# Kernel optimization log

Hardware: AMD Instinct MI355X
Metric: run time of the kernel (lower is better)

Reference implementation:

```python
import jax, jax.numpy as jnp
import numpy as np

# Mamba2 hyperparams (mamba_ssm defaults given __init__ args)
D_MODEL = 512
FF = 2048
D_STATE = 128
D_CONV = 4
EXPAND = 2
D_INNER = EXPAND * D_MODEL          # 1024
HEADDIM = 64
NHEADS = D_INNER // HEADDIM         # 16
NGROUPS = 1
CONV_DIM = D_INNER + 2 * NGROUPS * D_STATE       # 1280
D_IN_PROJ = 2 * D_INNER + 2 * NGROUPS * D_STATE + NHEADS  # 2320
CHUNK = 128
EPS = 1e-5


def setup_inputs() -> dict:
    key = jax.random.key(0)
    ks = jax.random.split(key, 16)
    B, S = 8, 2048
    s = 0.02
    dt_init = jax.random.uniform(ks[4], (NHEADS,), minval=0.001, maxval=0.1)
    return {
        # forward args (dropout treated as eval / identity)
        "tgt": jax.random.normal(ks[0], (B, S, D_MODEL), jnp.float32),
        "memory": jax.random.normal(ks[1], (B, 256, D_MODEL), jnp.float32),
        "spatial_shapes": jnp.array([[16, 16]], jnp.int32),
        "level_start_index": jnp.array([0], jnp.int32),
        "valid_ratios": jnp.ones((B, 1, 2), jnp.float32),
        # Mamba2 params
        "in_proj_w": jax.random.normal(ks[2], (D_IN_PROJ, D_MODEL), jnp.float32) * s,
        "conv_w": jax.random.normal(ks[3], (CONV_DIM, D_CONV), jnp.float32) * s,
        "conv_b": jnp.zeros((CONV_DIM,), jnp.float32),
        "dt_bias": jnp.log(jnp.expm1(dt_init)),  # inverse softplus of dt_init
        "A_log": jnp.log(jax.random.uniform(ks[5], (NHEADS,), minval=1.0, maxval=16.0)),
        "D_head": jnp.ones((NHEADS,), jnp.float32),
        "norm_w": jnp.ones((D_INNER,), jnp.float32),
        "out_proj_w": jax.random.normal(ks[6], (D_MODEL, D_INNER), jnp.float32) * s,
        # LayerNorms + FFN
        "norm1_w": jnp.ones((D_MODEL,)), "norm1_b": jnp.zeros((D_MODEL,)),
        "w1": jax.random.normal(ks[7], (FF, D_MODEL), jnp.float32) * s,
        "b1": jnp.zeros((FF,)),
        "w2": jax.random.normal(ks[8], (D_MODEL, FF), jnp.float32) * s,
        "b2": jnp.zeros((D_MODEL,)),
        "norm3_w": jnp.ones((D_MODEL,)), "norm3_b": jnp.zeros((D_MODEL,)),
    }


def _layer_norm(x, w, b):
    m = jnp.mean(x, -1, keepdims=True)
    v = jnp.mean((x - m) ** 2, -1, keepdims=True)
    return (x - m) * jax.lax.rsqrt(v + EPS) * w + b


def _ssd(x, dt, A, Bm, Cm):
    # chunked selective-scan (SSD). x:(b,s,h,p) dt:(b,s,h) A:(h,) Bm,Cm:(b,s,n)
    b, s, h, p = x.shape
    n = Bm.shape[-1]
    c, l = s // CHUNK, CHUNK
    x = x.reshape(b, c, l, h, p)
    dt = dt.reshape(b, c, l, h)
    Bm = Bm.reshape(b, c, l, n)
    Cm = Cm.reshape(b, c, l, n)
    a_cs = jnp.cumsum(dt * A, axis=2)                 # (b,c,l,h) cumulative log-decay
    ac = a_cs.transpose(0, 1, 3, 2)                   # (b,c,h,l)
    mask = jnp.tril(jnp.ones((l, l), bool))
    Lmat = jnp.exp(jnp.where(mask, ac[..., :, None] - ac[..., None, :], -jnp.inf))
    # intra-chunk (causal) contribution
    Y_diag = jnp.einsum('bcin,bcjn,bchij,bcjh,bcjhp->bcihp', Cm, Bm, Lmat, dt, x)
    # per-chunk final states
    decay_end = jnp.exp(a_cs[:, :, -1:, :] - a_cs)    # (b,c,l,h)
    states = jnp.einsum('bcln,bclh,bclh,bclhp->bchpn', Bm, decay_end, dt, x)
    chunk_decay = jnp.exp(a_cs[:, :, -1, :])          # (b,c,h)
    def step(h0, inp):
        cd, st = inp
        return cd[:, :, None, None] * h0 + st, h0
    h_init = jnp.zeros((b, h, p, n), x.dtype)
    _, prev = jax.lax.scan(step, h_init,
                           (chunk_decay.transpose(1, 0, 2),
                            states.transpose(1, 0, 2, 3, 4)))
    prev = prev.transpose(1, 0, 2, 3, 4)              # (b,c,h,p,n) state at chunk start
    Y_off = jnp.einsum('bcln,bchpn,bclh->bclhp', Cm, prev, jnp.exp(a_cs))
    return (Y_diag + Y_off).reshape(b, s, h, p)


def _mamba2(u, in_proj_w, conv_w, conv_b, dt_bias, A_log, D_head, norm_w, out_proj_w):
    Bb, S, _ = u.shape
    zxbcdt = u @ in_proj_w.T                          # (b,s,2320)
    z, xBC, dt = jnp.split(zxbcdt, [D_INNER, D_INNER + CONV_DIM], axis=-1)
    # causal depthwise conv1d + silu
    xp = jnp.pad(xBC, ((0, 0), (D_CONV - 1, 0), (0, 0)))
    conv = sum(xp[:, k:k + S, :] * conv_w[:, k] for k in range(D_CONV)) + conv_b
    xBC = jax.nn.silu(conv)
    x, Bm, Cm = jnp.split(xBC, [D_INNER, D_INNER + NGROUPS * D_STATE], axis=-1)
    dt = jax.nn.softplus(dt + dt_bias)                # (b,s,h)
    A = -jnp.exp(A_log)                               # (h,)
    x = x.reshape(Bb, S, NHEADS, HEADDIM)
    y = _ssd(x, dt, A, Bm, Cm) + D_head[None, None, :, None] * x
    y = y.reshape(Bb, S, D_INNER)
    # gated RMSNorm: rmsnorm(y * silu(z)) * w
    y = y * jax.nn.silu(z)
    y = y * jax.lax.rsqrt(jnp.mean(y * y, -1, keepdims=True) + EPS) * norm_w
    return y @ out_proj_w.T


def reference(tgt, memory, spatial_shapes, level_start_index, valid_ratios,
              in_proj_w, conv_w, conv_b, dt_bias, A_log, D_head, norm_w, out_proj_w,
              norm1_w, norm1_b, w1, b1, w2, b2, norm3_w, norm3_b):
    t2 = _mamba2(tgt, in_proj_w, conv_w, conv_b, dt_bias, A_log, D_head, norm_w, out_proj_w)
    t = _layer_norm(tgt + t2, norm1_w, norm1_b)
    ff = jax.nn.gelu(t @ w1.T + b1, approximate=False) @ w2.T + b2
    return _layer_norm(t + ff, norm3_w, norm3_b)
```

## Files before the change

### kernel.cpp

```cpp
#include <hip/hip_runtime.h>
#include <hip/hip_bf16.h>
#include <math.h>


namespace {
constexpr int BB = 8;
constexpr int S = 2048;
constexpr int DM = 512;
constexpr int DIP = 2320;
constexpr int DIPP = 2432;
constexpr int DI = 1024;
constexpr int CDIM = 1280;
constexpr int NH = 16;
constexpr int HD = 64;
constexpr int DSTATE = 128;
constexpr int CH = 128;
constexpr int NC = S / CH;
constexpr int FF = 2048;
constexpr float EPS = 1e-5f;
constexpr int LP = 132;
}

using bf16_t = __hip_bfloat16;
typedef __attribute__((ext_vector_type(8))) short short8;
typedef __attribute__((ext_vector_type(4))) float f32x4;

__device__ __forceinline__ float gelu_exact(float x) {
    return 0.5f * x * (1.0f + erff(x * 0.7071067811865476f));
}
__device__ __forceinline__ unsigned short f2bfu(float f) {
    bf16_t b = __float2bfloat16(f);
    return *(unsigned short*)&b;
}
__device__ __forceinline__ float bfu2f(unsigned short u) {
    union { unsigned int i; float f; } v; v.i = (unsigned)u << 16; return v.f;
}

__device__ __forceinline__ void gload16(const bf16_t* g, bf16_t* l) {
    __builtin_amdgcn_global_load_lds(
        (const __attribute__((address_space(1))) void*)g,
        (__attribute__((address_space(3))) void*)l, 16, 0, 0);
}

__device__ __forceinline__ void block_sum2(float& a, float& b) {
    #pragma unroll
    for (int o = 32; o > 0; o >>= 1) {
        a += __shfl_down(a, o, 64);
        b += __shfl_down(b, o, 64);
    }
    __shared__ float sa[4], sb[4];
    int w = threadIdx.x >> 6;
    if ((threadIdx.x & 63) == 0) { sa[w] = a; sb[w] = b; }
    __syncthreads();
    a = sa[0] + sa[1] + sa[2] + sa[3];
    b = sb[0] + sb[1] + sb[2] + sb[3];
}

template <int BM, int ACT, bool HASBIAS, bool OUTBF>
__global__ __launch_bounds__(256)
void mfma_gemm(const bf16_t* __restrict__ A, const bf16_t* __restrict__ W,
               const float* __restrict__ bias, void* __restrict__ Cout,
               int N, int K, int lda, int ldw, int ldc,
               long batchA, long batchW, long batchC)
{
    A += (long)blockIdx.z * batchA;
    W += (long)blockIdx.z * batchW;
    constexpr int NJ = (BM == 128) ? 4 : 2;
    __shared__ bf16_t As[2][BM * 32];
    __shared__ bf16_t Ws[2][4096];
    const int tid = threadIdx.x;
    const int lane = tid & 63;
    const int wave = tid >> 6;
    const long bm = (long)blockIdx.y * BM;
    const int bn = blockIdx.x * 128;

    const int rA = tid & (BM - 1);
    const int qA = tid / BM;
    const int rW = tid & 127;
    const int qW = tid >> 7;
    const bf16_t* Ag = A + (bm + rA) * (long)lda + qA * 8;
    const bf16_t* Wg = W + ((long)bn + rW) * (long)ldw + qW * 8;
    const int wbase = wave * 512;

    const int kq = lane >> 4;
    const int lr = lane & 15;
    const int wm = (BM == 128) ? (wave & 1) * 64 : 0;
    const int wn = (BM == 128) ? (wave >> 1) * 64 : wave * 32;

    f32x4 acc[4][NJ];
    #pragma unroll
    for (int i = 0; i < 4; i++)
        #pragma unroll
        for (int j = 0; j < NJ; j++) acc[i][j] = (f32x4){0.f, 0.f, 0.f, 0.f};

    {
        gload16(Ag, &As[0][wbase]);
        if (BM == 128) gload16(Ag + 16, &As[0][wbase + 2048]);
        gload16(Wg, &Ws[0][wbase]);
        gload16(Wg + 16, &Ws[0][wbase + 2048]);
    }
    __syncthreads();

    const int nt = K / 32;
    for (int t = 0; t < nt; t++) {
        const int cur = t & 1, nxt = cur ^ 1;
        if (t + 1 < nt) {
            const int ko = (t + 1) * 32;
            gload16(Ag + ko, &As[nxt][wbase]);
            if (BM == 128) gload16(Ag + ko + 16, &As[nxt][wbase + 2048]);
            gload16(Wg + ko, &Ws[nxt][wbase]);
            gload16(Wg + ko + 16, &Ws[nxt][wbase + 2048]);
        }
        short8 af[4], bfr[NJ];
        #pragma unroll
        for (int i = 0; i < 4; i++)
            af[i] = *(const short8*)&As[cur][(kq * BM + wm + i * 16 + lr) * 8];
        #pragma unroll
        for (int j = 0; j < NJ; j++)
            bfr[j] = *(const short8*)&Ws[cur][(kq * 128 + wn + j * 16 + lr) * 8];
        #pragma unroll
        for (int i = 0; i < 4; i++)
            #pragma unroll
            for (int j = 0; j < NJ; j++)
                acc[i][j] = __builtin_amdgcn_mfma_f32_16x16x32_bf16(af[i], bfr[j], acc[i][j], 0, 0, 0);
        __syncthreads();
    }

    #pragma unroll
    for (int i = 0; i < 4; i++) {
        #pragma unroll
        for (int j = 0; j < NJ; j++) {
            int col = bn + wn + j * 16 + lr;
            if (col < N) {
                float bv = HASBIAS ? bias[col] : 0.f;
                #pragma unroll
                for (int r = 0; r < 4; r++) {
                    long row = bm + wm + i * 16 + kq * 4 + r;
                    float v = acc[i][j][r] + bv;
                    if (ACT == 1) v = gelu_exact(v);
                    if (OUTBF) ((bf16_t*)Cout)[row * (long)ldc + col + blockIdx.z * batchC] = __float2bfloat16(v);
                    else       ((float*)Cout)[row * (long)ldc + col + blockIdx.z * batchC] = v;
                }
            }
        }
    }
}

template <int ACT, bool HASBIAS>
__global__ __launch_bounds__(256)
void gemm_kernel(const float* __restrict__ A, const float* __restrict__ W,
                 const float* __restrict__ bias, float* __restrict__ C,
                 int M, int N, int K, int lda, int ldw, int ldc,
                 long batchA, long batchW, long batchC)
{
    A += (long)blockIdx.z * batchA;
    W += (long)blockIdx.z * batchW;
    C += (long)blockIdx.z * batchC;
    __shared__ __align__(16) float Asm[16][68];
    __shared__ __align__(16) float Wsm[16][68];
    const int tid = threadIdx.x;
    const int bm = blockIdx.y * 64;
    const int bn = blockIdx.x * 64;
    const int tm = (tid & 15) * 4;
    const int tn = (tid >> 4) * 4;
    const int lr = tid >> 2;
    const int lk = (tid & 3) * 4;
    const float* Ap = A + (long)(bm + lr) * lda + lk;
    const float* Wp = W + (long)(bn + lr) * ldw + lk;
    const bool wv_ok = (bn + lr) < N;
    float acc[4][4];
    #pragma unroll
    for (int i = 0; i < 4; i++)
        #pragma unroll
        for (int j = 0; j < 4; j++) acc[i][j] = 0.f;

    for (int k0 = 0; k0 < K; k0 += 16) {
        float4 av = *(const float4*)(Ap + k0);
        float4 wv = wv_ok ? *(const float4*)(Wp + k0) : make_float4(0.f, 0.f, 0.f, 0.f);
        Asm[lk + 0][lr] = av.x; Asm[lk + 1][lr] = av.y;
        Asm[lk + 2][lr] = av.z; Asm[lk + 3][lr] = av.w;
        Wsm[lk + 0][lr] = wv.x; Wsm[lk + 1][lr] = wv.y;
        Wsm[lk + 2][lr] = wv.z; Wsm[lk + 3][lr] = wv.w;
        __syncthreads();
        #pragma unroll
        for (int k = 0; k < 16; k++) {
            float4 a = *(const float4*)&Asm[k][tm];
            float4 w = *(const float4*)&Wsm[k][tn];
            acc[0][0] += a.x * w.x; acc[0][1] += a.x * w.y; acc[0][2] += a.x * w.z; acc[0][3] += a.x * w.w;
            acc[1][0] += a.y * w.x; acc[1][1] += a.y * w.y; acc[1][2] += a.y * w.z; acc[1][3] += a.y * w.w;
            acc[2][0] += a.z * w.x; acc[2][1] += a.z * w.y; acc[2][2] += a.z * w.z; acc[2][3] += a.z * w.w;
            acc[3][0] += a.w * w.x; acc[3][1] += a.w * w.y; acc[3][2] += a.w * w.z; acc[3][3] += a.w * w.w;
        }
        __syncthreads();
    }
    #pragma unroll
    for (int i = 0; i < 4; i++) {
        long row = bm + tm + i;
        #pragma unroll
        for (int j = 0; j < 4; j++) {
            int col = bn + tn + j;
            if (col < N) {
                float v = acc[i][j];
                if (HASBIAS) v += bias[col];
                if (ACT == 1) v = gelu_exact(v);
                if (ACT == 2) v = (v > 20.f) ? v : log1pf(__expf(v));
                C[row * ldc + col] = v;
            }
        }
    }
}

__global__ __launch_bounds__(256)
void cvt_bf16(const float* __restrict__ s, bf16_t* __restrict__ d, long n)
{
    long i = ((long)blockIdx.x * 256 + threadIdx.x) * 4;
    if (i >= n) return;
    float4 v = *(const float4*)(s + i);
    d[i + 0] = __float2bfloat16(v.x);
    d[i + 1] = __float2bfloat16(v.y);
    d[i + 2] = __float2bfloat16(v.z);
    d[i + 3] = __float2bfloat16(v.w);
}

__global__ __launch_bounds__(256)
void cvt_bf16_pad(const float* __restrict__ s, bf16_t* __restrict__ d,
                  int rows_src, long total, int cols)
{
    long i = (long)blockIdx.x * 256 + threadIdx.x;
    if (i >= total) return;
    long r = i / cols;
    d[i] = __float2bfloat16(r < rows_src ? s[i] : 0.f);
}

__global__ __launch_bounds__(256)
void conv_silu_t16(const bf16_t* __restrict__ zx, const float* __restrict__ cw,
                   const float* __restrict__ cb, bf16_t* __restrict__ xBC)
{
    const int quad = blockIdx.x * 64 + (threadIdx.x & 63);
    const int wv = threadIdx.x >> 6;
    const int c = quad * 4;
    const int s0 = blockIdx.y * 64 + wv * 16;
    const long t0 = (long)blockIdx.z * S + s0;

    float wgt[4][4];
    #pragma unroll
    for (int cc = 0; cc < 4; cc++)
        #pragma unroll
        for (int k = 0; k < 4; k++) wgt[cc][k] = cw[(c + cc) * 4 + k];
    float bias[4];
    #pragma unroll
    for (int cc = 0; cc < 4; cc++) bias[cc] = cb[c + cc];

    unsigned long long rows[19];
    #pragma unroll
    for (int i = 0; i < 19; i++) {
        int s = s0 + i - 3;
        rows[i] = (s >= 0) ? *(const unsigned long long*)&zx[(t0 + i - 3) * DIP + DI + c] : 0ULL;
    }
    #pragma unroll
    for (int i = 0; i < 16; i++) {
        float v[4];
        #pragma unroll
        for (int cc = 0; cc < 4; cc++) v[cc] = bias[cc];
        #pragma unroll
        for (int k = 0; k < 4; k++) {
            unsigned long long u = rows[i + k];
            v[0] += bfu2f((unsigned short)(u      )) * wgt[0][k];
            v[1] += bfu2f((unsigned short)(u >> 16)) * wgt[1][k];
            v[2] += bfu2f((unsigned short)(u >> 32)) * wgt[2][k];
            v[3] += bfu2f((unsigned short)(u >> 48)) * wgt[3][k];
        }
        unsigned long long o = 0;
        #pragma unroll
        for (int cc = 0; cc < 4; cc++) {
            float sv = v[cc] / (1.f + __expf(-v[cc]));
            o |= (unsigned long long)f2bfu(sv) << (16 * cc);
        }
        *(unsigned long long*)&xBC[(t0 + i) * (long)CDIM + c] = o;
    }
}

__global__ __launch_bounds__(256)
void ssd_states(const bf16_t* __restrict__ xBC, const float* __restrict__ dts,
                const float* __restrict__ A_log,
                float* __restrict__ st, float* __restrict__ acs_all,
                float* __restrict__ cdlog)
{
    const int bid = blockIdx.x;
    const int nh = bid & 1;
    const int h = (bid >> 1) & 15;
    const int c = (bid >> 5) & 15;
    const int b = bid >> 9;
    const int sbid = (b * NC + c) * NH + h;
    const int tid = threadIdx.x;
    const int lane = tid & 63;
    const int wave = tid >> 6;
    __shared__ float dtv[128];
    __shared__ float acs[128];
    __shared__ float wj[128];
    __shared__ bf16_t XT[64 * LP];
    __shared__ bf16_t BwT[64 * LP];
    const long t0 = (long)b * S + (long)c * CH;
    const float Ah = -__expf(A_log[h]);

    if (tid < 128) {
        float d = dts[(t0 + tid) * NH + h];
        dtv[tid] = d;
        acs[tid] = d * Ah;
    }
    __syncthreads();
    for (int off = 1; off < 128; off <<= 1) {
        float add = 0.f;
        if (tid < 128 && tid >= off) add = acs[tid - off];
        __syncthreads();
        if (tid < 128 && tid >= off) acs[tid] += add;
        __syncthreads();
    }
    const float el = acs[127];
    if (tid < 128) wj[tid] = __expf(el - acs[tid]) * dtv[tid];
    if (nh == 0) {
        if (tid < 128) acs_all[(long)sbid * 128 + tid] = acs[tid];
        if (tid == 0) cdlog[sbid] = el;
    }
    __syncthreads();

    const int n0b = nh * 64;
    for (int i = tid; i < 4096; i += 256) {
        int p = i & 63, jp = (i >> 6) << 1;
        unsigned short a = *(const unsigned short*)&xBC[(t0 + jp) * CDIM + h * HD + p];
        unsigned short bb = *(const unsigned short*)&xBC[(t0 + jp + 1) * CDIM + h * HD + p];
        *(unsigned int*)&XT[p * LP + jp] = (unsigned)a | ((unsigned)bb << 16);
    }
    for (int i = tid; i < 4096; i += 256) {
        int n = i & 63, jp = (i >> 6) << 1;
        float v0 = __bfloat162float(xBC[(t0 + jp) * CDIM + DI + n0b + n]) * wj[jp];
        float v1 = __bfloat162float(xBC[(t0 + jp + 1) * CDIM + DI + n0b + n]) * wj[jp + 1];
        *(unsigned int*)&BwT[n * LP + jp] = (unsigned)f2bfu(v0) | ((unsigned)f2bfu(v1) << 16);
    }
    __syncthreads();

    const int kq = lane >> 4;
    const int lr = lane & 15;
    const int p0w = (wave & 1) * 32;
    const int n0w = (wave >> 1) * 32;
    f32x4 acc[2][2];
    #pragma unroll
    for (int i = 0; i < 2; i++)
        #pragma unroll
        for (int j = 0; j < 2; j++) acc[i][j] = (f32x4){0.f, 0.f, 0.f, 0.f};
    #pragma unroll
    for (int t = 0; t < 4; t++) {
        short8 af[2], bfr[2];
        #pragma unroll
        for (int i = 0; i < 2; i++)
            af[i] = *(const short8*)&XT[(p0w + i * 16 + lr) * LP + t * 32 + kq * 8];
        #pragma unroll
        for (int j = 0; j < 2; j++)
            bfr[j] = *(const short8*)&BwT[(n0w + j * 16 + lr) * LP + t * 32 + kq * 8];
        #pragma unroll
        for (int i = 0; i < 2; i++)
            #pragma unroll
            for (int j = 0; j < 2; j++)
                acc[i][j] = __builtin_amdgcn_mfma_f32_16x16x32_bf16(af[i], bfr[j], acc[i][j], 0, 0, 0);
    }
    long base = (long)sbid * 8192;
    #pragma unroll
    for (int i = 0; i < 2; i++)
        #pragma unroll
        for (int j = 0; j < 2; j++) {
            int col = n0b + n0w + j * 16 + lr;
            #pragma unroll
            for (int r = 0; r < 4; r++) {
                int p = p0w + i * 16 + kq * 4 + r;
                st[base + p * 128 + col] = acc[i][j][r];
            }
        }
}

__global__ __launch_bounds__(256)
void ssd_scan(float* __restrict__ st, const float* __restrict__ cdlog)
{
    const int h = blockIdx.x & 15;
    const int b = blockIdx.x >> 4;
    const int q0 = blockIdx.y * 8;
    const int tid = threadIdx.x;
    float prev[8];
    #pragma unroll
    for (int q = 0; q < 8; q++) prev[q] = 0.f;
    for (int c = 0; c < NC; c++) {
        int bc = (b * NC + c) * NH + h;
        float cd = __expf(cdlog[bc]);
        long base = (long)bc * 8192 + (long)q0 * 256;
        #pragma unroll
        for (int q = 0; q < 8; q++) {
            long idx = base + (long)q * 256 + tid;
            float v = st[idx];
            st[idx] = prev[q];
            prev[q] = cd * prev[q] + v;
        }
    }
}

__global__ __launch_bounds__(256)
void ssd_out(const bf16_t* __restrict__ xBC, const float* __restrict__ dts,
             const bf16_t* __restrict__ G, const float* __restrict__ st,
             const float* __restrict__ acs_all, const float* __restrict__ D_head,
             bf16_t* __restrict__ y)
{
    const int bid = blockIdx.x;
    const int ih = bid & 1;
    const int h = (bid >> 1) & 15;
    const int c = (bid >> 5) & 15;
    const int b = bid >> 9;
    const int sbid = (b * NC + c) * NH + h;
    const int tid = threadIdx.x;
    const int lane = tid & 63;
    const int wave = tid >> 6;
    __shared__ float dtv[128];
    __shared__ float acs[128];
    __shared__ float eacs[64];
    __shared__ bf16_t Abuf[64 * LP];
    __shared__ bf16_t Bbuf[64 * LP];
    const long t0 = (long)b * S + (long)c * CH;
    const int m0b = ih * 64;

    if (tid < 128) {
        dtv[tid] = dts[(t0 + tid) * NH + h];
        acs[tid] = acs_all[(long)sbid * 128 + tid];
    }
    __syncthreads();
    if (tid < 64) eacs[tid] = __expf(acs[m0b + tid]);

    const bf16_t* Gb = G + (long)(b * NC + c) * 128 * 128;
    for (int i = tid; i < 4096; i += 256) {
        int rl = i >> 6, kp = (i & 63) << 1;
        int grow = m0b + rl;
        unsigned int g2 = *(const unsigned int*)&Gb[grow * 128 + kp];
        float w0 = (kp     <= grow) ? bfu2f((unsigned short)(g2      )) * __expf(acs[grow] - acs[kp    ]) * dtv[kp    ] : 0.f;
        float w1 = (kp + 1 <= grow) ? bfu2f((unsigned short)(g2 >> 16)) * __expf(acs[grow] - acs[kp + 1]) * dtv[kp + 1] : 0.f;
        *(unsigned int*)&Abuf[rl * LP + kp] = (unsigned)f2bfu(w0) | ((unsigned)f2bfu(w1) << 16);
    }
    for (int i = tid; i < 4096; i += 256) {
        int p = i & 63, jp = (i >> 6) << 1;
        unsigned short a = *(const unsigned short*)&xBC[(t0 + jp) * CDIM + h * HD + p];
        unsigned short bb = *(const unsigned short*)&xBC[(t0 + jp + 1) * CDIM + h * HD + p];
        *(unsigned int*)&Bbuf[p * LP + jp] = (unsigned)a | ((unsigned)bb << 16);
    }
    __syncthreads();

    const int kq = lane >> 4;
    const int lr = lane & 15;
    const int m0w = (wave & 1) * 32;
    const int p0 = (wave >> 1) * 32;
    f32x4 acc[2][2];
    #pragma unroll
    for (int i = 0; i < 2; i++)
        #pragma unroll
        for (int j = 0; j < 2; j++) acc[i][j] = (f32x4){0.f, 0.f, 0.f, 0.f};

    #pragma unroll
    for (int t = 0; t < 4; t++) {
        short8 af[2], bfr[2];
        #pragma unroll
        for (int i = 0; i < 2; i++)
            af[i] = *(const short8*)&Abuf[(m0w + i * 16 + lr) * LP + t * 32 + kq * 8];
        #pragma unroll
        for (int j = 0; j < 2; j++)
            bfr[j] = *(const short8*)&Bbuf[(p0 + j * 16 + lr) * LP + t * 32 + kq * 8];
        #pragma unroll
        for (int i = 0; i < 2; i++)
            #pragma unroll
            for (int j = 0; j < 2; j++)
                acc[i][j] = __builtin_amdgcn_mfma_f32_16x16x32_bf16(af[i], bfr[j], acc[i][j], 0, 0, 0);
    }
    const float Dh = D_head[h];
    float dx[2][2][4];
    #pragma unroll
    for (int i = 0; i < 2; i++)
        #pragma unroll
        for (int j = 0; j < 2; j++) {
            int col = p0 + j * 16 + lr;
            #pragma unroll
            for (int r = 0; r < 4; r++) {
                int rl = m0w + i * 16 + kq * 4 + r;
                dx[i][j][r] = Dh * __bfloat162float(Bbuf[col * LP + m0b + rl]);
            }
        }
    __syncthreads();

    for (int i = tid; i < 4096; i += 256) {
        int rl = i >> 6, np = (i & 63) << 1;
        unsigned int c2 = *(const unsigned int*)&xBC[(t0 + m0b + rl) * CDIM + DI + DSTATE + np];
        float e = eacs[rl];
        float v0 = e * bfu2f((unsigned short)(c2      ));
        float v1 = e * bfu2f((unsigned short)(c2 >> 16));
        *(unsigned int*)&Abuf[rl * LP + np] = (unsigned)f2bfu(v0) | ((unsigned)f2bfu(v1) << 16);
    }
    for (int i = tid; i < 4096; i += 256) {
        int p = i >> 6, np = (i & 63) << 1;
        float2 v = *(const float2*)&st[(long)sbid * 8192 + p * 128 + np];
        *(unsigned int*)&Bbuf[p * LP + np] = (unsigned)f2bfu(v.x) | ((unsigned)f2bfu(v.y) << 16);
    }
    __syncthreads();

    #pragma unroll
    for (int t = 0; t < 4; t++) {
        short8 af[2], bfr[2];
        #pragma unroll
        for (int i = 0; i < 2; i++)
            af[i] = *(const short8*)&Abuf[(m0w + i * 16 + lr) * LP + t * 32 + kq * 8];
        #pragma unroll
        for (int j = 0; j < 2; j++)
            bfr[j] = *(const short8*)&Bbuf[(p0 + j * 16 + lr) * LP + t * 32 + kq * 8];
        #pragma unroll
        for (int i = 0; i < 2; i++)
            #pragma unroll
            for (int j = 0; j < 2; j++)
                acc[i][j] = __builtin_amdgcn_mfma_f32_16x16x32_bf16(af[i], bfr[j], acc[i][j], 0, 0, 0);
    }

    #pragma unroll
    for (int i = 0; i < 2; i++)
        #pragma unroll
        for (int j = 0; j < 2; j++) {
            int col = p0 + j * 16 + lr;
            #pragma unroll
            for (int r = 0; r < 4; r++) {
                int rl = m0w + i * 16 + kq * 4 + r;
                y[(t0 + m0b + rl) * DI + h * HD + col] = __float2bfloat16(acc[i][j][r] + dx[i][j][r]);
            }
        }
}

__global__ __launch_bounds__(256)
void gated_rms(const bf16_t* __restrict__ y, const bf16_t* __restrict__ zx,
               const float* __restrict__ norm_w, bf16_t* __restrict__ yn)
{
    const long t = blockIdx.x;
    const int d = threadIdx.x * 4;
    unsigned long long zu = *(const unsigned long long*)&zx[t * DIP + d];
    unsigned long long yu = *(const unsigned long long*)&y[t * DI + d];
    float g[4];
    float ss = 0.f, dummy = 0.f;
    #pragma unroll
    for (int q = 0; q < 4; q++) {
        float zv = bfu2f((unsigned short)(zu >> (16 * q)));
        float yv = bfu2f((unsigned short)(yu >> (16 * q)));
        float gv = yv * (zv / (1.f + __expf(-zv)));
        g[q] = gv;
        ss += gv * gv;
    }
    block_sum2(ss, dummy);
    float scale = rsqrtf(ss * (1.f / DI) + EPS);
    unsigned long long o = 0;
    #pragma unroll
    for (int q = 0; q < 4; q++)
        o |= (unsigned long long)f2bfu(g[q] * scale * norm_w[d + q]) << (16 * q);
    *(unsigned long long*)&yn[t * DI + d] = o;
}

template <bool W16>
__global__ __launch_bounds__(256)
void add_ln(const float* __restrict__ x, const float* __restrict__ r,
            const float* __restrict__ w, const float* __restrict__ bpar,
            float* __restrict__ o32, bf16_t* __restrict__ o16)
{
    const int tid = threadIdx.x;
    const long t = blockIdx.x * 2 + (tid >> 7);
    const int i = (tid & 127) * 4;
    float4 xv = *(const float4*)(x + t * DM + i);
    float4 rv = *(const float4*)(r + t * DM + i);
    float v[4] = {xv.x + rv.x, xv.y + rv.y, xv.z + rv.z, xv.w + rv.w};
    float s = v[0] + v[1] + v[2] + v[3];
    float s2 = v[0]*v[0] + v[1]*v[1] + v[2]*v[2] + v[3]*v[3];
    #pragma unroll
    for (int o = 32; o > 0; o >>= 1) {
        s += __shfl_down(s, o, 64);
        s2 += __shfl_down(s2, o, 64);
    }
    __shared__ float sa[4], sb[4];
    int wv = tid >> 6;
    if ((tid & 63) == 0) { sa[wv] = s; sb[wv] = s2; }
    __syncthreads();
    int base = (tid >> 7) * 2;
    s = sa[base] + sa[base + 1];
    s2 = sb[base] + sb[base + 1];
    float mean = s * (1.f / DM);
    float var = s2 * (1.f / DM) - mean * mean;
    float inv = rsqrtf(var + EPS);
    float4 ov;
    float* op = (float*)&ov;
    unsigned long long o16u = 0;
    #pragma unroll
    for (int q = 0; q < 4; q++) {
        float o = (v[q] - mean) * inv * w[i + q] + bpar[i + q];
        op[q] = o;
        if (W16) o16u |= (unsigned long long)f2bfu(o) << (16 * q);
    }
    *(float4*)(o32 + t * DM + i) = ov;
    if (W16) *(unsigned long long*)&o16[t * DM + i] = o16u;
}


extern "C" void kernel_launch(void* const* d_in, const int* in_sizes, int n_in,
                              void* d_out, int out_size, void* d_ws, size_t ws_size,
                              hipStream_t stream)
{
    const float* tgt       = (const float*)d_in[0];
    const float* in_proj_w = (const float*)d_in[5];
    const float* conv_w    = (const float*)d_in[6];
    const float* conv_b    = (const float*)d_in[7];
    const float* dt_bias   = (const float*)d_in[8];
    const float* A_log     = (const float*)d_in[9];
    const float* D_head    = (const float*)d_in[10];
    const float* norm_w    = (const float*)d_in[11];
    const float* out_proj_w= (const float*)d_in[12];
    const float* norm1_w   = (const float*)d_in[13];
    const float* norm1_b   = (const float*)d_in[14];
    const float* w1        = (const float*)d_in[15];
    const float* b1        = (const float*)d_in[16];
    const float* w2        = (const float*)d_in[17];
    const float* b2        = (const float*)d_in[18];
    const float* norm3_w   = (const float*)d_in[19];
    const float* norm3_b   = (const float*)d_in[20];
    float* out = (float*)d_out;

    float* ws = (float*)d_ws;

    const size_t SZ_INW  = (size_t)DIPP * DM / 2;
    const size_t SZ_OUTW = (size_t)DM * DI / 2;
    const size_t SZ_W1   = (size_t)FF * DM / 2;
    const size_t SZ_W2   = (size_t)DM * FF / 2;
    size_t wo = 0;
    bf16_t* inW  = (bf16_t*)(ws + wo); wo += SZ_INW;
    bf16_t* outW = (bf16_t*)(ws + wo); wo += SZ_OUTW;
    bf16_t* w1b  = (bf16_t*)(ws + wo); wo += SZ_W1;
    bf16_t* w2b  = (bf16_t*)(ws + wo); wo += SZ_W2;
    const size_t WB = wo;

    const size_t PB = (size_t)S * DM / 2
                    + (size_t)S * DIP / 2
                    + (size_t)S * NH
                    + (size_t)S * CDIM / 2
                    + (size_t)NC * 128 * 128 / 2
                    + (size_t)NC * NH * 128
                    + (size_t)NC * NH
                    + (size_t)S * DI
                    + (size_t)S * DI;
    int NB = 0;
    for (int nb = 8; nb >= 1; nb >>= 1) {
        if (ws_size >= (WB + (size_t)nb * PB) * sizeof(float)) { NB = nb; break; }
    }
    if (NB == 0) return;

    {
        long n = (long)DIPP * DM;
        cvt_bf16_pad<<<(n + 255) / 256, 256, 0, stream>>>(in_proj_w, inW, DIP, n, DM);
        n = (long)DM * DI;
        cvt_bf16<<<(n / 4 + 255) / 256, 256, 0, stream>>>(out_proj_w, outW, n);
        n = (long)FF * DM;
        cvt_bf16<<<(n / 4 + 255) / 256, 256, 0, stream>>>(w1, w1b, n);
        n = (long)DM * FF;
        cvt_bf16<<<(n / 4 + 255) / 256, 256, 0, stream>>>(w2, w2b, n);
    }

    for (int b0 = 0; b0 < BB; b0 += NB) {
        const long Tg = (long)NB * S;
        size_t o = WB;
        bf16_t* tgt_bf = (bf16_t*)(ws + o); o += (size_t)Tg * DM / 2;
        bf16_t* zx     = (bf16_t*)(ws + o); o += (size_t)Tg * DIP / 2;
        float*  dts    = ws + o;            o += (size_t)Tg * NH;
        bf16_t* xBC    = (bf16_t*)(ws + o); o += (size_t)Tg * CDIM / 2;
        bf16_t* Gbuf   = (bf16_t*)(ws + o); o += (size_t)NB * NC * 128 * 128 / 2;
        float*  acs    = ws + o;            o += (size_t)NB * NC * NH * 128;
        float*  cdl    = ws + o;            o += (size_t)NB * NC * NH;
        float*  ybuf   = ws + o;            o += (size_t)Tg * DI;
        float*  st     = ws + o;            o += (size_t)Tg * DI;

        bf16_t* ybf = (bf16_t*)ybuf;
        bf16_t* yn  = (bf16_t*)st;
        float*  t2  = ybuf;
        float*  tb  = (float*)zx;
        bf16_t* tbb = (bf16_t*)(((float*)zx) + Tg * DM);
        bf16_t* h1  = (bf16_t*)ybuf;
        float*  fb  = (float*)xBC;

        const float* tgt_g = tgt + (long)b0 * S * DM;
        float* out_g = out + (long)b0 * S * DM;

        cvt_bf16<<<((Tg * DM) / 4 + 255) / 256, 256, 0, stream>>>(tgt_g, tgt_bf, Tg * DM);
        mfma_gemm<128, 0, false, true><<<dim3(DIPP / 128, Tg / 128, 1), 256, 0, stream>>>(
            tgt_bf, inW, nullptr, zx, DIP, DM, DM, DM, DIP, 0, 0, 0);
        gemm_kernel<2, true><<<dim3(1, Tg / 64, 1), 256, 0, stream>>>(
            tgt_g, in_proj_w + (long)(DI + CDIM) * DM, dt_bias, dts,
            Tg, NH, DM, DM, DM, NH, 0, 0, 0);
        conv_silu_t16<<<dim3(CDIM / 256, S / 64, NB), 256, 0, stream>>>(zx, conv_w, conv_b, xBC);
        mfma_gemm<128, 0, false, true><<<dim3(1, 1, NB * NC), 256, 0, stream>>>(
            xBC + DI + DSTATE, xBC + DI, nullptr, Gbuf,
            128, DSTATE, CDIM, CDIM, 128,
            (long)CH * CDIM, (long)CH * CDIM, (long)128 * 128);
        ssd_states<<<NB * NC * NH * 2, 256, 0, stream>>>(xBC, dts, A_log, st, acs, cdl);
        ssd_scan<<<dim3(NB * NH, 4), 256, 0, stream>>>(st, cdl);
        ssd_out<<<NB * NC * NH * 2, 256, 0, stream>>>(xBC, dts, Gbuf, st, acs, D_head, ybf);
        gated_rms<<<Tg, 256, 0, stream>>>(ybf, zx, norm_w, yn);
        mfma_gemm<64, 0, false, false><<<dim3(DM / 128, Tg / 64, 1), 256, 0, stream>>>(
            yn, outW, nullptr, t2, DM, DI, DI, DI, DM, 0, 0, 0);
        add_ln<true><<<Tg / 2, 256, 0, stream>>>(tgt_g, t2, norm1_w, norm1_b, tb, tbb);
        mfma_gemm<128, 1, true, true><<<dim3(FF / 128, Tg / 128, 1), 256, 0, stream>>>(
            tbb, w1b, b1, h1, FF, DM, DM, DM, FF, 0, 0, 0);
        mfma_gemm<64, 0, true, false><<<dim3(DM / 128, Tg / 64, 1), 256, 0, stream>>>(
            h1, w2b, b2, fb, DM, FF, FF, FF, DM, 0, 0, 0);
        add_ln<false><<<Tg / 2, 256, 0, stream>>>(tb, fb, norm3_w, norm3_b, out_g, nullptr);
    }
}
```

Baseline: 855.4 us.

## Register-staged GEMM pipeline, fused dt projection with bf16 cast, bf16 scan states

The MFMA GEMM stops using global_load_lds and instead prefetches the next K-tile into registers, storing it to LDS after the current tile's compute, with a configurable BK (64 for the out-proj and FFN2 GEMMs, which also move to 128-row tiles). The scalar fp32 dt GEMM and the separate tgt-to-bf16 conversion kernel are merged into one warp-reduction kernel. The SSD scan now writes inter-chunk states as bf16 into a separate buffer, so ssd_out reads half the bytes and skips the conversion. Together these cut launches and memory traffic and aim to hide load latency, at the cost of more registers and LDS per block and fewer blocks for the N=512 GEMMs.

```diff
diff --git a/kernel.cpp b/kernel.cpp
--- a/kernel.cpp
+++ b/kernel.cpp
@@ -36,12 +36,6 @@
     union { unsigned int i; float f; } v; v.i = (unsigned)u << 16; return v.f;
 }
 
-__device__ __forceinline__ void gload16(const bf16_t* g, bf16_t* l) {
-    __builtin_amdgcn_global_load_lds(
-        (const __attribute__((address_space(1))) void*)g,
-        (__attribute__((address_space(3))) void*)l, 16, 0, 0);
-}
-
 __device__ __forceinline__ void block_sum2(float& a, float& b) {
     #pragma unroll
     for (int o = 32; o > 0; o >>= 1) {
@@ -56,7 +50,7 @@
     b = sb[0] + sb[1] + sb[2] + sb[3];
 }
 
-template <int BM, int ACT, bool HASBIAS, bool OUTBF>
+template <int BM, int BK, int ACT, bool HASBIAS, bool OUTBF>
 __global__ __launch_bounds__(256)
 void mfma_gemm(const bf16_t* __restrict__ A, const bf16_t* __restrict__ W,
                const float* __restrict__ bias, void* __restrict__ Cout,
@@ -66,8 +60,12 @@
     A += (long)blockIdx.z * batchA;
     W += (long)blockIdx.z * batchW;
     constexpr int NJ = (BM == 128) ? 4 : 2;
-    __shared__ bf16_t As[2][BM * 32];
-    __shared__ bf16_t Ws[2][4096];
+    constexpr int KO = BK / 32;
+    constexpr int QA = 256 / BM;
+    constexpr int TA = (BM * BK) / 2048;
+    constexpr int TW = (128 * BK) / 2048;
+    __shared__ bf16_t As[2][BM * BK];
+    __shared__ bf16_t Ws[2][128 * BK];
     const int tid = threadIdx.x;
     const int lane = tid & 63;
     const int wave = tid >> 6;
@@ -80,7 +78,8 @@
     const int qW = tid >> 7;
     const bf16_t* Ag = A + (bm + rA) * (long)lda + qA * 8;
     const bf16_t* Wg = W + ((long)bn + rW) * (long)ldw + qW * 8;
-    const int wbase = wave * 512;
+    const int laoff = (qA * BM + rA) * 8;
+    const int lwoff = (qW * 128 + rW) * 8;
 
     const int kq = lane >> 4;
     const int lr = lane & 15;
@@ -93,37 +92,48 @@
         #pragma unroll
         for (int j = 0; j < NJ; j++) acc[i][j] = (f32x4){0.f, 0.f, 0.f, 0.f};
 
-    {
-        gload16(Ag, &As[0][wbase]);
-        if (BM == 128) gload16(Ag + 16, &As[0][wbase + 2048]);
-        gload16(Wg, &Ws[0][wbase]);
-        gload16(Wg + 16, &Ws[0][wbase + 2048]);
-    }
-    __syncthreads();
-
-    const int nt = K / 32;
+    short8 ra[TA], rw[TW];
+    #pragma unroll
+    for (int u = 0; u < TA; u++) ra[u] = *(const short8*)(Ag + u * (QA * 8));
+    #pragma unroll
+    for (int u = 0; u < TW; u++) rw[u] = *(const short8*)(Wg + u * 16);
+    #pragma unroll
+    for (int u = 0; u < TA; u++) *(short8*)&As[0][laoff + u * (QA * BM * 8)] = ra[u];
+    #pragma unroll
+    for (int u = 0; u < TW; u++) *(short8*)&Ws[0][lwoff + u * 2048] = rw[u];
+
+    const int nt = K / BK;
     for (int t = 0; t < nt; t++) {
         const int cur = t & 1, nxt = cur ^ 1;
         if (t + 1 < nt) {
-            const int ko = (t + 1) * 32;
-            gload16(Ag + ko, &As[nxt][wbase]);
-            if (BM == 128) gload16(Ag + ko + 16, &As[nxt][wbase + 2048]);
-            gload16(Wg + ko, &Ws[nxt][wbase]);
-            gload16(Wg + ko + 16, &Ws[nxt][wbase + 2048]);
-        }
-        short8 af[4], bfr[NJ];
-        #pragma unroll
-        for (int i = 0; i < 4; i++)
-            af[i] = *(const short8*)&As[cur][(kq * BM + wm + i * 16 + lr) * 8];
-        #pragma unroll
-        for (int j = 0; j < NJ; j++)
-            bfr[j] = *(const short8*)&Ws[cur][(kq * 128 + wn + j * 16 + lr) * 8];
-        #pragma unroll
-        for (int i = 0; i < 4; i++)
+            const long ko = (long)(t + 1) * BK;
+            #pragma unroll
+            for (int u = 0; u < TA; u++) ra[u] = *(const short8*)(Ag + ko + u * (QA * 8));
+            #pragma unroll
+            for (int u = 0; u < TW; u++) rw[u] = *(const short8*)(Wg + ko + u * 16);
+        }
+        __syncthreads();
+        #pragma unroll
+        for (int hk = 0; hk < KO; hk++) {
+            short8 af[4], bfr[NJ];
+            #pragma unroll
+            for (int i = 0; i < 4; i++)
+                af[i] = *(const short8*)&As[cur][((hk * 4 + kq) * BM + wm + i * 16 + lr) * 8];
             #pragma unroll
             for (int j = 0; j < NJ; j++)
-                acc[i][j] = __builtin_amdgcn_mfma_f32_16x16x32_bf16(af[i], bfr[j], acc[i][j], 0, 0, 0);
-        __syncthreads();
+                bfr[j] = *(const short8*)&Ws[cur][((hk * 4 + kq) * 128 + wn + j * 16 + lr) * 8];
+            #pragma unroll
+            for (int i = 0; i < 4; i++)
+                #pragma unroll
+                for (int j = 0; j < NJ; j++)
+                    acc[i][j] = __builtin_amdgcn_mfma_f32_16x16x32_bf16(af[i], bfr[j], acc[i][j], 0, 0, 0);
+        }
+        if (t + 1 < nt) {
+            #pragma unroll
+            for (int u = 0; u < TA; u++) *(short8*)&As[nxt][laoff + u * (QA * BM * 8)] = ra[u];
+            #pragma unroll
+            for (int u = 0; u < TW; u++) *(short8*)&Ws[nxt][lwoff + u * 2048] = rw[u];
+        }
     }
 
     #pragma unroll
@@ -146,65 +156,55 @@
     }
 }
 
-template <int ACT, bool HASBIAS>
-__global__ __launch_bounds__(256)
-void gemm_kernel(const float* __restrict__ A, const float* __restrict__ W,
-                 const float* __restrict__ bias, float* __restrict__ C,
-                 int M, int N, int K, int lda, int ldw, int ldc,
-                 long batchA, long batchW, long batchC)
-{
-    A += (long)blockIdx.z * batchA;
-    W += (long)blockIdx.z * batchW;
-    C += (long)blockIdx.z * batchC;
-    __shared__ __align__(16) float Asm[16][68];
-    __shared__ __align__(16) float Wsm[16][68];
-    const int tid = threadIdx.x;
-    const int bm = blockIdx.y * 64;
-    const int bn = blockIdx.x * 64;
-    const int tm = (tid & 15) * 4;
-    const int tn = (tid >> 4) * 4;
-    const int lr = tid >> 2;
-    const int lk = (tid & 3) * 4;
-    const float* Ap = A + (long)(bm + lr) * lda + lk;
-    const float* Wp = W + (long)(bn + lr) * ldw + lk;
-    const bool wv_ok = (bn + lr) < N;
-    float acc[4][4];
-    #pragma unroll
-    for (int i = 0; i < 4; i++)
-        #pragma unroll
-        for (int j = 0; j < 4; j++) acc[i][j] = 0.f;
-
-    for (int k0 = 0; k0 < K; k0 += 16) {
-        float4 av = *(const float4*)(Ap + k0);
-        float4 wv = wv_ok ? *(const float4*)(Wp + k0) : make_float4(0.f, 0.f, 0.f, 0.f);
-        Asm[lk + 0][lr] = av.x; Asm[lk + 1][lr] = av.y;
-        Asm[lk + 2][lr] = av.z; Asm[lk + 3][lr] = av.w;
-        Wsm[lk + 0][lr] = wv.x; Wsm[lk + 1][lr] = wv.y;
-        Wsm[lk + 2][lr] = wv.z; Wsm[lk + 3][lr] = wv.w;
-        __syncthreads();
-        #pragma unroll
-        for (int k = 0; k < 16; k++) {
-            float4 a = *(const float4*)&Asm[k][tm];
-            float4 w = *(const float4*)&Wsm[k][tn];
-            acc[0][0] += a.x * w.x; acc[0][1] += a.x * w.y; acc[0][2] += a.x * w.z; acc[0][3] += a.x * w.w;
-            acc[1][0] += a.y * w.x; acc[1][1] += a.y * w.y; acc[1][2] += a.y * w.z; acc[1][3] += a.y * w.w;
-            acc[2][0] += a.z * w.x; acc[2][1] += a.z * w.y; acc[2][2] += a.z * w.z; acc[2][3] += a.z * w.w;
-            acc[3][0] += a.w * w.x; acc[3][1] += a.w * w.y; acc[3][2] += a.w * w.z; acc[3][3] += a.w * w.w;
-        }
-        __syncthreads();
-    }
-    #pragma unroll
-    for (int i = 0; i < 4; i++) {
-        long row = bm + tm + i;
-        #pragma unroll
-        for (int j = 0; j < 4; j++) {
-            int col = bn + tn + j;
-            if (col < N) {
-                float v = acc[i][j];
-                if (HASBIAS) v += bias[col];
-                if (ACT == 1) v = gelu_exact(v);
-                if (ACT == 2) v = (v > 20.f) ? v : log1pf(__expf(v));
-                C[row * ldc + col] = v;
+__global__ __launch_bounds__(256)
+void dt_cvt(const float* __restrict__ tgt, const float* __restrict__ Wdt,
+            const float* __restrict__ dt_bias, bf16_t* __restrict__ tgt_bf,
+            float* __restrict__ dts)
+{
+    const int lane = threadIdx.x & 63;
+    const int wave = threadIdx.x >> 6;
+    float Wl[16][8];
+    #pragma unroll
+    for (int h = 0; h < 16; h++) {
+        float4 a = *(const float4*)&Wdt[h * 512 + lane * 8];
+        float4 b = *(const float4*)&Wdt[h * 512 + lane * 8 + 4];
+        Wl[h][0] = a.x; Wl[h][1] = a.y; Wl[h][2] = a.z; Wl[h][3] = a.w;
+        Wl[h][4] = b.x; Wl[h][5] = b.y; Wl[h][6] = b.z; Wl[h][7] = b.w;
+    }
+    float bs[16];
+    #pragma unroll
+    for (int h = 0; h < 16; h++) bs[h] = dt_bias[h];
+
+    const long row0 = ((long)blockIdx.x * 4 + wave) * 4;
+    #pragma unroll
+    for (int rr = 0; rr < 4; rr++) {
+        const long t = row0 + rr;
+        float4 xa = *(const float4*)&tgt[t * 512 + lane * 8];
+        float4 xb = *(const float4*)&tgt[t * 512 + lane * 8 + 4];
+        float x[8] = {xa.x, xa.y, xa.z, xa.w, xb.x, xb.y, xb.z, xb.w};
+        short8 ob;
+        #pragma unroll
+        for (int q = 0; q < 8; q++) ob[q] = (short)f2bfu(x[q]);
+        *(short8*)&tgt_bf[t * 512 + lane * 8] = ob;
+
+        float acc[16];
+        #pragma unroll
+        for (int h = 0; h < 16; h++) {
+            float s = 0.f;
+            #pragma unroll
+            for (int q = 0; q < 8; q++) s += x[q] * Wl[h][q];
+            acc[h] = s;
+        }
+        #pragma unroll
+        for (int off = 32; off > 0; off >>= 1)
+            #pragma unroll
+            for (int h = 0; h < 16; h++)
+                acc[h] += __shfl_xor(acc[h], off, 64);
+        if (lane == 0) {
+            #pragma unroll
+            for (int h = 0; h < 16; h++) {
+                float v = acc[h] + bs[h];
+                dts[t * NH + h] = (v > 20.f) ? v : log1pf(__expf(v));
             }
         }
     }
@@ -378,7 +378,8 @@
 }
 
 __global__ __launch_bounds__(256)
-void ssd_scan(float* __restrict__ st, const float* __restrict__ cdlog)
+void ssd_scan(const float* __restrict__ st, const float* __restrict__ cdlog,
+              bf16_t* __restrict__ prevb)
 {
     const int h = blockIdx.x & 15;
     const int b = blockIdx.x >> 4;
@@ -395,7 +396,7 @@
         for (int q = 0; q < 8; q++) {
             long idx = base + (long)q * 256 + tid;
             float v = st[idx];
-            st[idx] = prev[q];
+            prevb[idx] = __float2bfloat16(prev[q]);
             prev[q] = cd * prev[q] + v;
         }
     }
@@ -403,7 +404,7 @@
 
 __global__ __launch_bounds__(256)
 void ssd_out(const bf16_t* __restrict__ xBC, const float* __restrict__ dts,
-             const bf16_t* __restrict__ G, const float* __restrict__ st,
+             const bf16_t* __restrict__ G, const bf16_t* __restrict__ prevb,
              const float* __restrict__ acs_all, const float* __restrict__ D_head,
              bf16_t* __restrict__ y)
 {
@@ -498,8 +499,8 @@
     }
     for (int i = tid; i < 4096; i += 256) {
         int p = i >> 6, np = (i & 63) << 1;
-        float2 v = *(const float2*)&st[(long)sbid * 8192 + p * 128 + np];
-        *(unsigned int*)&Bbuf[p * LP + np] = (unsigned)f2bfu(v.x) | ((unsigned)f2bfu(v.y) << 16);
+        *(unsigned int*)&Bbuf[p * LP + np] =
+            *(const unsigned int*)&prevb[(long)sbid * 8192 + p * 128 + np];
     }
     __syncthreads();
 
@@ -677,7 +678,8 @@
         float*  ybuf   = ws + o;            o += (size_t)Tg * DI;
         float*  st     = ws + o;            o += (size_t)Tg * DI;
 
-        bf16_t* ybf = (bf16_t*)ybuf;
+        bf16_t* ybf   = (bf16_t*)ybuf;
+        bf16_t* prevb = (bf16_t*)(ybuf + (size_t)Tg * DI / 2);
         bf16_t* yn  = (bf16_t*)st;
         float*  t2  = ybuf;
         float*  tb  = (float*)zx;
@@ -688,27 +690,25 @@
         const float* tgt_g = tgt + (long)b0 * S * DM;
         float* out_g = out + (long)b0 * S * DM;
 
-        cvt_bf16<<<((Tg * DM) / 4 + 255) / 256, 256, 0, stream>>>(tgt_g, tgt_bf, Tg * DM);
-        mfma_gemm<128, 0, false, true><<<dim3(DIPP / 128, Tg / 128, 1), 256, 0, stream>>>(
+        dt_cvt<<<Tg / 16, 256, 0, stream>>>(
+            tgt_g, in_proj_w + (long)(DI + CDIM) * DM, dt_bias, tgt_bf, dts);
+        mfma_gemm<128, 32, 0, false, true><<<dim3(DIPP / 128, Tg / 128, 1), 256, 0, stream>>>(
             tgt_bf, inW, nullptr, zx, DIP, DM, DM, DM, DIP, 0, 0, 0);
-        gemm_kernel<2, true><<<dim3(1, Tg / 64, 1), 256, 0, stream>>>(
-            tgt_g, in_proj_w + (long)(DI + CDIM) * DM, dt_bias, dts,
-            Tg, NH, DM, DM, DM, NH, 0, 0, 0);
         conv_silu_t16<<<dim3(CDIM / 256, S / 64, NB), 256, 0, stream>>>(zx, conv_w, conv_b, xBC);
-        mfma_gemm<128, 0, false, true><<<dim3(1, 1, NB * NC), 256, 0, stream>>>(
+        mfma_gemm<128, 32, 0, false, true><<<dim3(1, 1, NB * NC), 256, 0, stream>>>(
             xBC + DI + DSTATE, xBC + DI, nullptr, Gbuf,
             128, DSTATE, CDIM, CDIM, 128,
             (long)CH * CDIM, (long)CH * CDIM, (long)128 * 128);
         ssd_states<<<NB * NC * NH * 2, 256, 0, stream>>>(xBC, dts, A_log, st, acs, cdl);
-        ssd_scan<<<dim3(NB * NH, 4), 256, 0, stream>>>(st, cdl);
-        ssd_out<<<NB * NC * NH * 2, 256, 0, stream>>>(xBC, dts, Gbuf, st, acs, D_head, ybf);
+        ssd_scan<<<dim3(NB * NH, 4), 256, 0, stream>>>(st, cdl, prevb);
+        ssd_out<<<NB * NC * NH * 2, 256, 0, stream>>>(xBC, dts, Gbuf, prevb, acs, D_head, ybf);
         gated_rms<<<Tg, 256, 0, stream>>>(ybf, zx, norm_w, yn);
-        mfma_gemm<64, 0, false, false><<<dim3(DM / 128, Tg / 64, 1), 256, 0, stream>>>(
+        mfma_gemm<128, 64, 0, false, false><<<dim3(DM / 128, Tg / 128, 1), 256, 0, stream>>>(
             yn, outW, nullptr, t2, DM, DI, DI, DI, DM, 0, 0, 0);
         add_ln<true><<<Tg / 2, 256, 0, stream>>>(tgt_g, t2, norm1_w, norm1_b, tb, tbb);
-        mfma_gemm<128, 1, true, true><<<dim3(FF / 128, Tg / 128, 1), 256, 0, stream>>>(
+        mfma_gemm<128, 32, 1, true, true><<<dim3(FF / 128, Tg / 128, 1), 256, 0, stream>>>(
             tbb, w1b, b1, h1, FF, DM, DM, DM, FF, 0, 0, 0);
-        mfma_gemm<64, 0, true, false><<<dim3(DM / 128, Tg / 64, 1), 256, 0, stream>>>(
+        mfma_gemm<128, 64, 0, true, false><<<dim3(DM / 128, Tg / 128, 1), 256, 0, stream>>>(
             h1, w2b, b2, fb, DM, FF, FF, FF, DM, 0, 0, 0);
         add_ln<false><<<Tg / 2, 256, 0, stream>>>(tb, fb, norm3_w, norm3_b, out_g, nullptr);
     }
```

Result: faster. 795.0 us (median of 3 runs) (-7.1%).
